# Optimization experiments

Measured on AMD Instinct MI355X. Metric: run time of the kernel, lower is better.

## Reference

```python
import math
import jax, jax.numpy as jnp
import numpy as np

EPS = 1e-5
RATIO = 0.5


def gcn_conv(x, src, dst, ew, W, b):
    # GCNConv(add_self_loops=True, normalize=True, improved=True): self-loop fill = 2.0
    N = x.shape[0]
    h = x @ W  # [N, Cout]
    deg = jax.ops.segment_sum(ew, dst, num_segments=N) + 2.0
    dinv = jnp.where(deg > 0, deg ** -0.5, 0.0)
    norm = dinv[src] * ew * dinv[dst]  # [E]
    agg = jax.ops.segment_sum(h[src] * norm[:, None], dst, num_segments=N)
    return agg + (2.0 * dinv * dinv)[:, None] * h + b


def batch_norm(x, g, b):
    # training-mode BatchNorm1d over nodes (biased variance)
    mu = x.mean(0)
    var = x.var(0)
    return (x - mu) * jax.lax.rsqrt(var + EPS) * g + b


def topk_pool(x, src, dst, ew, p):
    # TopKPooling: score = tanh(x.p/||p||), keep top ceil(ratio*N), x' = x[perm]*score[perm]
    N = x.shape[0]
    k = int(math.ceil(RATIO * N))
    score = jnp.tanh((x @ p) / jnp.linalg.norm(p))
    vals, perm = jax.lax.top_k(score, k)
    xk = x[perm] * vals[:, None]
    new_idx = jnp.full((N,), -1, jnp.int32).at[perm].set(jnp.arange(k, dtype=jnp.int32))
    ns, nd = new_idx[src], new_idx[dst]
    keep = (ns >= 0) & (nd >= 0)
    # keep fixed edge count; dropped edges get weight 0 -> contribute nothing
    return xk, jnp.where(keep, ns, 0), jnp.where(keep, nd, 0), jnp.where(keep, ew, 0.0), perm


def encode(x, src, dst, ew, mW, mb, g1, b1, cW, cb, g2, b2):
    x = batch_norm(jax.nn.relu(x @ mW + mb), g1, b1)  # MLP: Lin -> ReLU -> BN
    x = gcn_conv(x, src, dst, ew, cW, cb)
    return jax.nn.relu(batch_norm(x, g2, b2))


def unet(x, edge_src, edge_dst,
         e0_mlp_W, e0_mlp_b, e0_bn1_g, e0_bn1_b, e0_conv_W, e0_conv_b, e0_n_g, e0_n_b,
         e1_p, e1_mlp_W, e1_mlp_b, e1_bn1_g, e1_bn1_b, e1_conv_W, e1_conv_b, e1_n_g, e1_n_b,
         e2_p, e2_mlp_W, e2_mlp_b, e2_bn1_g, e2_bn1_b, e2_conv_W, e2_conv_b, e2_n_g, e2_n_b,
         d2_W, d2_b, d1_W, d1_b, d0_W, d0_b):
    E = edge_src.shape[0]
    ew0 = jnp.ones((E,), x.dtype)
    # encoder0 (no pool)
    x1 = encode(x, edge_src, edge_dst, ew0, e0_mlp_W, e0_mlp_b, e0_bn1_g, e0_bn1_b,
                e0_conv_W, e0_conv_b, e0_n_g, e0_n_b)
    # encoder1 (pool 0.5)
    xp, s1, t1, ew1, perm1 = topk_pool(x1, edge_src, edge_dst, ew0, e1_p)
    x2 = encode(xp, s1, t1, ew1, e1_mlp_W, e1_mlp_b, e1_bn1_g, e1_bn1_b,
                e1_conv_W, e1_conv_b, e1_n_g, e1_n_b)
    # encoder2 (pool 0.5)
    xp, s2, t2, ew2, perm2 = topk_pool(x2, s1, t1, ew1, e2_p)
    x3 = encode(xp, s2, t2, ew2, e2_mlp_W, e2_mlp_b, e2_bn1_g, e2_bn1_b,
                e2_conv_W, e2_conv_b, e2_n_g, e2_n_b)
    # decoder2 + unpool into x2 via perm2: up[perm]=(x+res[perm])/2, up[~perm]=res
    d = jax.nn.relu(gcn_conv(x3, s2, t2, ew2, d2_W, d2_b))
    xu = x2.at[perm2].set((d + x2[perm2]) * 0.5)
    # decoder1 + unpool into x1 via perm1
    d = jax.nn.relu(gcn_conv(xu, s1, t1, ew1, d1_W, d1_b))
    xu = x1.at[perm1].set((d + x1[perm1]) * 0.5)
    # decoder0 on the original graph, no activation
    return gcn_conv(xu, edge_src, edge_dst, ew0, d0_W, d0_b)


def setup_inputs() -> dict:
    key = jax.random.key(0)
    N, E, C = 100000, 1600000, [16, 64, 128, 256]
    ks = iter(jax.random.split(key, 64))
    nk = lambda: next(ks)

    def glorot(shape):
        s = math.sqrt(6.0 / (shape[0] + shape[1]))
        return jax.random.uniform(nk(), shape, minval=-s, maxval=s, dtype=jnp.float32)

    inp = {
        'x': jax.random.normal(nk(), (N, C[0]), jnp.float32),
        'edge_src': jax.random.randint(nk(), (E,), 0, N, jnp.int32),
        'edge_dst': jax.random.randint(nk(), (E,), 0, N, jnp.int32),
    }
    for i, (ci, co) in enumerate(zip(C[:-1], C[1:])):
        pre = f'e{i}_'
        if i > 0:
            inp[pre + 'p'] = jax.random.normal(nk(), (ci,), jnp.float32)
        inp[pre + 'mlp_W'] = glorot((ci, co)); inp[pre + 'mlp_b'] = jnp.zeros((co,), jnp.float32)
        inp[pre + 'bn1_g'] = jnp.ones((co,), jnp.float32); inp[pre + 'bn1_b'] = jnp.zeros((co,), jnp.float32)
        inp[pre + 'conv_W'] = glorot((co, co)); inp[pre + 'conv_b'] = jnp.zeros((co,), jnp.float32)
        inp[pre + 'n_g'] = jnp.ones((co,), jnp.float32); inp[pre + 'n_b'] = jnp.zeros((co,), jnp.float32)
    inp['d2_W'] = glorot((256, 128)); inp['d2_b'] = jnp.zeros((128,), jnp.float32)
    inp['d1_W'] = glorot((128, 64)); inp['d1_b'] = jnp.zeros((64,), jnp.float32)
    inp['d0_W'] = glorot((64, 16)); inp['d0_b'] = jnp.zeros((16,), jnp.float32)
    return inp


def reference(x, edge_src, edge_dst,
              e0_mlp_W, e0_mlp_b, e0_bn1_g, e0_bn1_b, e0_conv_W, e0_conv_b, e0_n_g, e0_n_b,
              e1_p, e1_mlp_W, e1_mlp_b, e1_bn1_g, e1_bn1_b, e1_conv_W, e1_conv_b, e1_n_g, e1_n_b,
              e2_p, e2_mlp_W, e2_mlp_b, e2_bn1_g, e2_bn1_b, e2_conv_W, e2_conv_b, e2_n_g, e2_n_b,
              d2_W, d2_b, d1_W, d1_b, d0_W, d0_b):
    return unet(x, edge_src, edge_dst,
                e0_mlp_W, e0_mlp_b, e0_bn1_g, e0_bn1_b, e0_conv_W, e0_conv_b, e0_n_g, e0_n_b,
                e1_p, e1_mlp_W, e1_mlp_b, e1_bn1_g, e1_bn1_b, e1_conv_W, e1_conv_b, e1_n_g, e1_n_b,
                e2_p, e2_mlp_W, e2_mlp_b, e2_bn1_g, e2_bn1_b, e2_conv_W, e2_conv_b, e2_n_g, e2_n_b,
                d2_W, d2_b, d1_W, d1_b, d0_W, d0_b)
```

## Files before the change

### kernel.cpp

```cpp
#include <hip/hip_runtime.h>
#include <math.h>

static inline int cdiv(int a, int b){ return (a + b - 1) / b; }

#define SCAN_CHUNK 4096
#define BCHUNK 4096

typedef _Float16 v4h __attribute__((ext_vector_type(4)));
typedef float    v4f __attribute__((ext_vector_type(4)));


__global__ void k_count0(const int* __restrict__ dst, int* __restrict__ cnt, int E){
  int i = blockIdx.x*blockDim.x + threadIdx.x;
  if (i < E) atomicAdd(&cnt[dst[i]], 1);
}

__global__ __launch_bounds__(256) void k_bucket(const int* __restrict__ src, const int* __restrict__ dst,
                        int E, int* __restrict__ gcur, unsigned int* __restrict__ bout){
  __shared__ int lcnt[256], gbase[256];
  int t = threadIdx.x;
  lcnt[t] = 0;
  __syncthreads();
  int base = blockIdx.x*BCHUNK;
  int end = min(base + BCHUNK, E);
  for (int i = base + t; i < end; i += 256) atomicAdd(&lcnt[dst[i] >> 9], 1);
  __syncthreads();
  gbase[t] = lcnt[t] ? atomicAdd(&gcur[t], lcnt[t]) : 0;
  __syncthreads();
  lcnt[t] = 0;
  __syncthreads();
  for (int i = base + t; i < end; i += 256){
    int s = src[i], d = dst[i];
    int b = d >> 9;
    int pos = gbase[b] + atomicAdd(&lcnt[b], 1);
    bout[pos] = ((unsigned int)s << 9) | (unsigned int)(d & 511);
  }
}

__global__ __launch_bounds__(256) void k_fill_b(const unsigned int* __restrict__ bout,
                        const int* __restrict__ rowptr, int* __restrict__ fillg,
                        int* __restrict__ cols, int N, int BPB){
  int b = blockIdx.x / BPB, sub = blockIdx.x % BPB;
  int r0 = b << 9;
  int r1 = min(r0 + 512, N);
  int start = rowptr[r0], end = rowptr[r1];
  for (int i = start + sub*256 + threadIdx.x; i < end; i += BPB*256){
    unsigned int v = bout[i];
    int d = r0 + (int)(v & 511u);
    int pos = rowptr[d] + atomicAdd(&fillg[d], 1);
    cols[pos] = (int)(v >> 9);
  }
}

__global__ void k_count_csr(const int* __restrict__ rowptrA, const int* __restrict__ colsA,
                            const int* __restrict__ nidx, int* __restrict__ cnt, int NA){
  int n = blockIdx.x*blockDim.x + threadIdx.x;
  if (n >= NA) return;
  int m = nidx[n];
  if (m < 0) return;
  int c = 0;
  int je = rowptrA[n+1];
  for (int j = rowptrA[n]; j < je; ++j) c += (nidx[colsA[j]] >= 0);
  cnt[m] = c;
}

__global__ void k_fill_csr(const int* __restrict__ rowptrA, const int* __restrict__ colsA,
                           const int* __restrict__ nidx, const int* __restrict__ rowptrB,
                           int* __restrict__ colsB, int NA){
  int n = blockIdx.x*blockDim.x + threadIdx.x;
  if (n >= NA) return;
  int m = nidx[n];
  if (m < 0) return;
  int pos = rowptrB[m];
  int je = rowptrA[n+1];
  for (int j = rowptrA[n]; j < je; ++j){
    int s = nidx[colsA[j]];
    if (s >= 0) colsB[pos++] = s;
  }
}


__global__ __launch_bounds__(256) void k_scan_p1(const int* __restrict__ in, int nIn, int* __restrict__ bsum){
  __shared__ int sh[256];
  int base = blockIdx.x*SCAN_CHUNK;
  int end = min(base + SCAN_CHUNK, nIn);
  int s = 0;
  for (int i = base + threadIdx.x; i < end; i += 256) s += in[i];
  sh[threadIdx.x] = s; __syncthreads();
  for (int o = 128; o > 0; o >>= 1){
    if (threadIdx.x < o) sh[threadIdx.x] += sh[threadIdx.x + o];
    __syncthreads();
  }
  if (threadIdx.x == 0) bsum[blockIdx.x] = sh[0];
}

__global__ __launch_bounds__(256) void k_scan_p2(int* __restrict__ bsum, int nb){
  __shared__ int sh[256];
  int t = threadIdx.x;
  int v = (t < nb) ? bsum[t] : 0;
  sh[t] = v; __syncthreads();
  for (int o = 1; o < 256; o <<= 1){
    int u = (t >= o) ? sh[t-o] : 0;
    __syncthreads();
    sh[t] += u;
    __syncthreads();
  }
  if (t < nb) bsum[t] = sh[t] - v;
}

__global__ __launch_bounds__(256) void k_scan_p3(const int* __restrict__ cnt, const int* __restrict__ bsum,
                        int* __restrict__ rowptr, float* __restrict__ dinv,
                        int* __restrict__ gcur, int nIn){
  int t = threadIdx.x;
  int tb = blockIdx.x*SCAN_CHUNK + t*16;
  int my[16]; int s = 0;
#pragma unroll
  for (int j = 0; j < 16; ++j){
    int i = tb + j;
    int v = (i < nIn) ? cnt[i] : 0;
    my[j] = v; s += v;
  }
  __shared__ int sh[256];
  sh[t] = s; __syncthreads();
  for (int o = 1; o < 256; o <<= 1){
    int u = (t >= o) ? sh[t-o] : 0;
    __syncthreads();
    sh[t] += u;
    __syncthreads();
  }
  int run = bsum[blockIdx.x] + sh[t] - s;
#pragma unroll
  for (int j = 0; j < 16; ++j){
    int i = tb + j;
    if (i < nIn){
      rowptr[i] = run;
      if (dinv) dinv[i] = rsqrtf((float)my[j] + 2.0f);
      if (gcur && (i & 511) == 0) gcur[i >> 9] = run;
      run += my[j];
    } else if (i == nIn){
      rowptr[nIn] = run;
    }
  }
}


__global__ void k_prep_w_el(const float* __restrict__ W, const float* __restrict__ ss,
                            _Float16* __restrict__ Whi, _Float16* __restrict__ Wlo,
                            float* __restrict__ bias2, const float* __restrict__ bias,
                            int KM, int M, int mshift, int mmask){
  int idx = blockIdx.x*256 + threadIdx.x;
  if (idx >= KM) return;
  int k = idx >> mshift, m = idx & mmask;
  float w = W[idx];
  if (ss) w *= ss[k];
  _Float16 hi = (_Float16)w;
  size_t oidx = ((size_t)(k >> 2)*M + m)*4 + (k & 3);
  Whi[oidx] = hi;
  if (Wlo) Wlo[oidx] = (_Float16)(w - (float)hi);
  if (k == 0) bias2[m] = bias ? bias[m] : 0.f;
}

__global__ void k_prep_bias(const float* __restrict__ W, const float* __restrict__ ss,
                            float* __restrict__ bias2, int K, int M){
  int m = blockIdx.x;
  int lane = threadIdx.x;
  float s = 0.f;
  for (int k = lane; k < K; k += 64) s = fmaf(ss[K + k], W[(size_t)k*M + m], s);
  for (int o = 32; o > 0; o >>= 1) s += __shfl_down(s, o, 64);
  if (lane == 0) bias2[m] = s;
}


template<int SPLIT>
__global__ __launch_bounds__(256) void k_gemm16(
    const float* __restrict__ A, const _Float16* __restrict__ Whi,
    const _Float16* __restrict__ Wlo, const float* __restrict__ bias2,
    float* __restrict__ Out32, _Float16* __restrict__ Out16,
    float* __restrict__ stats, int N, int K, int M, int relu)
{
  __shared__ float sacc[64], s2acc[64];
  int tid = threadIdx.x;
  if (stats){
    if (tid < 64){ sacc[tid] = 0.f; s2acc[tid] = 0.f; }
    __syncthreads();
  }
  int wave = tid >> 6, lane = tid & 63;
  int g = lane >> 4, r = lane & 15;
  int wrow0 = blockIdx.x*256 + wave*64;
  int col0 = blockIdx.y*64;
  int nf = (M - col0) >> 4; if (nf > 4) nf = 4;
  v4f acc[4][4];
#pragma unroll
  for (int rt = 0; rt < 4; ++rt)
#pragma unroll
    for (int c = 0; c < 4; ++c) acc[rt][c] = (v4f){0.f,0.f,0.f,0.f};

  for (int k0 = 0; k0 < K; k0 += 16){
    int kb = (k0 >> 2) + g;
    v4h bh[4], bl[4];
#pragma unroll
    for (int c = 0; c < 4; ++c){
      if (c >= nf) continue;
      size_t bidx = ((size_t)kb*M + col0 + c*16 + r)*4;
      bh[c] = *(const v4h*)&Whi[bidx];
      if (SPLIT) bl[c] = *(const v4h*)&Wlo[bidx];
    }
    v4h ah[4], al[4];
#pragma unroll
    for (int rt = 0; rt < 4; ++rt){
      int arow = wrow0 + rt*16 + r;
      if (arow < N){
        float4 av = *(const float4*)&A[(size_t)arow*K + k0 + g*4];
        float xs[4] = {av.x, av.y, av.z, av.w};
#pragma unroll
        for (int j = 0; j < 4; ++j){
          _Float16 hi = (_Float16)xs[j];
          ah[rt][j] = hi;
          if (SPLIT) al[rt][j] = (_Float16)(xs[j] - (float)hi);
        }
      } else {
#pragma unroll
        for (int j = 0; j < 4; ++j){ ah[rt][j] = (_Float16)0.f; if (SPLIT) al[rt][j] = (_Float16)0.f; }
      }
    }
#pragma unroll
    for (int rt = 0; rt < 4; ++rt){
#pragma unroll
      for (int c = 0; c < 4; ++c){
        if (c >= nf) continue;
        acc[rt][c] = __builtin_amdgcn_mfma_f32_16x16x16f16(ah[rt], bh[c], acc[rt][c], 0, 0, 0);
        if (SPLIT){
          acc[rt][c] = __builtin_amdgcn_mfma_f32_16x16x16f16(al[rt], bh[c], acc[rt][c], 0, 0, 0);
          acc[rt][c] = __builtin_amdgcn_mfma_f32_16x16x16f16(ah[rt], bl[c], acc[rt][c], 0, 0, 0);
        }
      }
    }
  }

#pragma unroll
  for (int c = 0; c < 4; ++c){
    if (c >= nf) continue;
    int col = col0 + c*16 + r;
    float bsv = bias2[col];
    float s = 0.f, s2 = 0.f;
#pragma unroll
    for (int rt = 0; rt < 4; ++rt){
#pragma unroll
      for (int i = 0; i < 4; ++i){
        int rr = wrow0 + rt*16 + g*4 + i;
        float v = acc[rt][c][i] + bsv;
        if (relu) v = fmaxf(v, 0.f);
        if (rr < N){
          if (Out32) Out32[(size_t)rr*M + col] = v;
          if (Out16) Out16[(size_t)rr*M + col] = (_Float16)v;
          s += v; s2 = fmaf(v, v, s2);
        }
      }
    }
    if (stats){
      s  += __shfl_xor(s, 16);  s  += __shfl_xor(s, 32);
      s2 += __shfl_xor(s2, 16); s2 += __shfl_xor(s2, 32);
      if (g == 0){
        atomicAdd(&sacc[c*16 + r], s);
        atomicAdd(&s2acc[c*16 + r], s2);
      }
    }
  }
  if (stats){
    __syncthreads();
    if (tid < 64 && col0 + tid < M){
      atomicAdd(&stats[col0 + tid], sacc[tid]);
      atomicAdd(&stats[M + col0 + tid], s2acc[tid]);
    }
  }
}


__global__ void k_bn_stats(const float* __restrict__ X, float* __restrict__ acc, int N, int C){
  int col = threadIdx.x % C;
  int rg  = threadIdx.x / C;
  int R   = blockDim.x / C;
  float s = 0.f, s2 = 0.f;
  for (int r = blockIdx.x*R + rg; r < N; r += gridDim.x*R){
    float v = X[(size_t)r*C + col];
    s += v; s2 += v*v;
  }
  __shared__ float sh[256], sh2[256];
  sh[threadIdx.x] = s; sh2[threadIdx.x] = s2;
  __syncthreads();
  if (rg == 0){
    for (int r = 1; r < R; ++r){ s += sh[r*C + col]; s2 += sh2[r*C + col]; }
    atomicAdd(&acc[col], s);
    atomicAdd(&acc[C + col], s2);
  }
}

__global__ void k_bn_final(const float* __restrict__ acc, const float* __restrict__ g,
                           const float* __restrict__ b, float* __restrict__ ss, int N, int C){
  int c = threadIdx.x;
  if (c >= C) return;
  float mu  = acc[c] / (float)N;
  float var = acc[C + c] / (float)N - mu*mu;
  float sc  = rsqrtf(var + 1e-5f) * g[c];
  ss[c]     = sc;
  ss[C + c] = b[c] - mu*sc;
}

__global__ void k_bn_apply(const float* __restrict__ X, float* __restrict__ Y,
                           const float* __restrict__ ss, int total, int C, int relu){
  int i = blockIdx.x*blockDim.x + threadIdx.x;
  if (i >= total) return;
  int c = i % C;
  float v = X[i]*ss[c] + ss[C + c];
  if (relu) v = fmaxf(v, 0.f);
  Y[i] = v;
}


template<int C, typename T>
__global__ void k_agg(const T* __restrict__ h, const int* __restrict__ rowptr,
                      const int* __restrict__ cols, const float* __restrict__ dinv,
                      const float* __restrict__ bias, float* __restrict__ out,
                      int N, int relu)
{
  constexpr int TPN = (C < 64) ? C : 64;
  constexpr int R = C / TPN;
  int gid  = blockIdx.x*blockDim.x + threadIdx.x;
  int node = gid / TPN;
  int lane = gid % TPN;
  if (node >= N) return;
  float di = dinv[node];
  float acc[R];
#pragma unroll
  for (int r = 0; r < R; ++r) acc[r] = 0.f;
  int j  = rowptr[node];
  int je = rowptr[node+1];
  for (; j + 4 <= je; j += 4){
    int s0 = cols[j], s1 = cols[j+1], s2 = cols[j+2], s3 = cols[j+3];
    float w0 = dinv[s0]*di, w1 = dinv[s1]*di, w2 = dinv[s2]*di, w3 = dinv[s3]*di;
#pragma unroll
    for (int r = 0; r < R; ++r){
      float h0 = (float)h[(size_t)s0*C + lane + r*TPN];
      float h1 = (float)h[(size_t)s1*C + lane + r*TPN];
      float h2 = (float)h[(size_t)s2*C + lane + r*TPN];
      float h3 = (float)h[(size_t)s3*C + lane + r*TPN];
      acc[r] = fmaf(w0, h0, acc[r]);
      acc[r] = fmaf(w1, h1, acc[r]);
      acc[r] = fmaf(w2, h2, acc[r]);
      acc[r] = fmaf(w3, h3, acc[r]);
    }
  }
  for (; j < je; ++j){
    int s = cols[j];
    float wgt = dinv[s]*di;
#pragma unroll
    for (int r = 0; r < R; ++r)
      acc[r] = fmaf(wgt, (float)h[(size_t)s*C + lane + r*TPN], acc[r]);
  }
  float sw = 2.f*di*di;
#pragma unroll
  for (int r = 0; r < R; ++r){
    int c = lane + r*TPN;
    float v = acc[r] + sw*(float)h[(size_t)node*C + c] + bias[c];
    if (relu) v = fmaxf(v, 0.f);
    out[(size_t)node*C + c] = v;
  }
}

template<typename T>
static void launch_agg(const T* h, const int* rp, const int* cl, const float* dv,
                       const float* bias, float* o, int N, int C, int relu, hipStream_t stream){
  int tpn = (C < 64) ? C : 64;
  dim3 g(cdiv(N*tpn, 256));
  switch (C){
    case 16:  k_agg<16,T> <<<g, dim3(256), 0, stream>>>(h, rp, cl, dv, bias, o, N, relu); break;
    case 64:  k_agg<64,T> <<<g, dim3(256), 0, stream>>>(h, rp, cl, dv, bias, o, N, relu); break;
    case 128: k_agg<128,T><<<g, dim3(256), 0, stream>>>(h, rp, cl, dv, bias, o, N, relu); break;
    case 256: k_agg<256,T><<<g, dim3(256), 0, stream>>>(h, rp, cl, dv, bias, o, N, relu); break;
  }
}


__global__ void k_score(const float* __restrict__ X, const float* __restrict__ p,
                        float* __restrict__ val, unsigned int* __restrict__ key, int N, int C){
  int wid  = (blockIdx.x*blockDim.x + threadIdx.x) >> 6;
  int lane = threadIdx.x & 63;
  if (wid >= N) return;
  float s = 0.f, np = 0.f;
  for (int c = lane; c < C; c += 64){
    float pv = p[c];
    s = fmaf(X[(size_t)wid*C + c], pv, s);
    np = fmaf(pv, pv, np);
  }
  for (int o = 32; o > 0; o >>= 1){ s += __shfl_down(s, o, 64); np += __shfl_down(np, o, 64); }
  if (lane == 0){
    float sc = tanhf(s * rsqrtf(np));
    val[wid] = sc;
    unsigned int b = __float_as_uint(sc);
    key[wid] = (b & 0x80000000u) ? ~b : (b | 0x80000000u);
  }
}

__global__ void k_hist_hi(const unsigned int* __restrict__ key, int N, unsigned int* __restrict__ hist){
  int i = blockIdx.x*blockDim.x + threadIdx.x;
  if (i < N) atomicAdd(&hist[key[i] >> 16], 1u);
}

__global__ void k_hist_lo(const unsigned int* __restrict__ key, int N,
                          const int* __restrict__ state, unsigned int* __restrict__ hist){
  int i = blockIdx.x*blockDim.x + threadIdx.x;
  if (i >= N) return;
  unsigned int kk = key[i];
  if ((int)(kk >> 16) == state[1]) atomicAdd(&hist[kk & 0xffffu], 1u);
}

__global__ void k_scan_hist(unsigned int* __restrict__ hist, int* __restrict__ state,
                            int karg, int kidx, int bidx, int ridx){
  __shared__ unsigned int part[1024];
  __shared__ unsigned int suff[1024];
  int t = threadIdx.x;
  unsigned int s = 0;
  int base = t*64;
  for (int j = 0; j < 64; ++j) s += hist[base + j];
  part[t] = s;
  suff[t] = s;
  __syncthreads();
  for (int o = 1; o < 1024; o <<= 1){
    unsigned int v = (t + o < 1024) ? suff[t + o] : 0u;
    __syncthreads();
    suff[t] += v;
    __syncthreads();
  }
  unsigned int k = (unsigned int)((kidx >= 0) ? state[kidx] : karg);
  unsigned int above = suff[t] - part[t];
  if (above < k && above + part[t] >= k){
    unsigned int cum = above;
    for (int b = 63; b >= 0; --b){
      unsigned int c = hist[base + b];
      if (cum + c >= k){ state[bidx] = base + b; state[ridx] = (int)(k - cum); break; }
      cum += c;
    }
  }
  __syncthreads();
  for (int j = 0; j < 64; ++j) hist[base + j] = 0u;
}


__global__ __launch_bounds__(256) void k_sel_p1(const unsigned int* __restrict__ key, int n,
                       const int* __restrict__ state, int2* __restrict__ bcnt){
  unsigned int T = ((unsigned int)state[1] << 16) | (unsigned int)state[3];
  int base = blockIdx.x*SCAN_CHUNK;
  int end = min(base + SCAN_CHUNK, n);
  int gt = 0, eq = 0;
  for (int i = base + threadIdx.x; i < end; i += 256){
    unsigned int v = key[i];
    gt += (v > T); eq += (v == T);
  }
  __shared__ int sg[256], se[256];
  sg[threadIdx.x] = gt; se[threadIdx.x] = eq;
  __syncthreads();
  for (int o = 128; o > 0; o >>= 1){
    if (threadIdx.x < o){ sg[threadIdx.x] += sg[threadIdx.x + o]; se[threadIdx.x] += se[threadIdx.x + o]; }
    __syncthreads();
  }
  if (threadIdx.x == 0) bcnt[blockIdx.x] = make_int2(sg[0], se[0]);
}

__global__ __launch_bounds__(256) void k_sel_p2(int2* __restrict__ bcnt, int nb){
  __shared__ int sg[256], se[256];
  int t = threadIdx.x;
  int2 v = (t < nb) ? bcnt[t] : make_int2(0, 0);
  sg[t] = v.x; se[t] = v.y; __syncthreads();
  for (int o = 1; o < 256; o <<= 1){
    int a = (t >= o) ? sg[t-o] : 0;
    int b = (t >= o) ? se[t-o] : 0;
    __syncthreads();
    sg[t] += a; se[t] += b;
    __syncthreads();
  }
  if (t < nb) bcnt[t] = make_int2(sg[t] - v.x, se[t] - v.y);
}

__global__ __launch_bounds__(256) void k_sel_p3(const unsigned int* __restrict__ key, int n,
                       const int* __restrict__ state, const int2* __restrict__ bcnt,
                       int* __restrict__ nidx){
  unsigned int T = ((unsigned int)state[1] << 16) | (unsigned int)state[3];
  int m = state[4];
  int t = threadIdx.x;
  int tb = blockIdx.x*SCAN_CHUNK + t*16;
  unsigned int kk[16];
  int gt = 0, eq = 0;
#pragma unroll
  for (int j = 0; j < 16; ++j){
    int i = tb + j;
    bool ok = i < n;
    unsigned int v = ok ? key[i] : 0u;
    kk[j] = v;
    gt += (ok && v > T); eq += (ok && v == T);
  }
  __shared__ unsigned long long sh[256];
  unsigned long long mine = ((unsigned long long)(unsigned)gt << 32) | (unsigned)eq;
  sh[t] = mine; __syncthreads();
  for (int o = 1; o < 256; o <<= 1){
    unsigned long long u = (t >= o) ? sh[t-o] : 0ull;
    __syncthreads();
    sh[t] += u;
    __syncthreads();
  }
  unsigned long long excl = sh[t] - mine;
  int2 bo = bcnt[blockIdx.x];
  int gb = bo.x + (int)(excl >> 32);
  int eb = bo.y + (int)(excl & 0xffffffffu);
#pragma unroll
  for (int j = 0; j < 16; ++j){
    int i = tb + j;
    if (i >= n) break;
    unsigned int v = kk[j];
    bool g = v > T, e = v == T;
    bool sel = g || (e && eb < m);
    nidx[i] = sel ? (gb + (eb < m ? eb : m)) : -1;
    gb += g; eb += e;
  }
}

__global__ void k_pool(const float* __restrict__ X, const float* __restrict__ val,
                       const int* __restrict__ nidx, float* __restrict__ Y, int N, int C){
  int i = blockIdx.x*blockDim.x + threadIdx.x;
  int n = i / C, c = i % C;
  if (n >= N) return;
  int m = nidx[n];
  if (m >= 0) Y[(size_t)m*C + c] = X[i]*val[n];
}

__global__ void k_unpool(float* __restrict__ X, const float* __restrict__ D,
                         const int* __restrict__ nidx, int N, int C){
  int i = blockIdx.x*blockDim.x + threadIdx.x;
  int n = i / C, c = i % C;
  if (n >= N) return;
  int m = nidx[n];
  if (m >= 0) X[i] = (D[(size_t)m*C + c] + X[i])*0.5f;
}


extern "C" void kernel_launch(void* const* d_in, const int* in_sizes, int n_in,
                              void* d_out, int out_size, void* d_ws, size_t ws_size,
                              hipStream_t stream)
{
  const float* x_in = (const float*)d_in[0];
  const int*   esrc = (const int*)d_in[1];
  const int*   edst = (const int*)d_in[2];
  const float* e0_mlp_W = (const float*)d_in[3];
  const float* e0_mlp_b = (const float*)d_in[4];
  const float* e0_bn1_g = (const float*)d_in[5];
  const float* e0_bn1_b = (const float*)d_in[6];
  const float* e0_conv_W= (const float*)d_in[7];
  const float* e0_conv_b= (const float*)d_in[8];
  const float* e0_n_g   = (const float*)d_in[9];
  const float* e0_n_b   = (const float*)d_in[10];
  const float* e1_p     = (const float*)d_in[11];
  const float* e1_mlp_W = (const float*)d_in[12];
  const float* e1_mlp_b = (const float*)d_in[13];
  const float* e1_bn1_g = (const float*)d_in[14];
  const float* e1_bn1_b = (const float*)d_in[15];
  const float* e1_conv_W= (const float*)d_in[16];
  const float* e1_conv_b= (const float*)d_in[17];
  const float* e1_n_g   = (const float*)d_in[18];
  const float* e1_n_b   = (const float*)d_in[19];
  const float* e2_p     = (const float*)d_in[20];
  const float* e2_mlp_W = (const float*)d_in[21];
  const float* e2_mlp_b = (const float*)d_in[22];
  const float* e2_bn1_g = (const float*)d_in[23];
  const float* e2_bn1_b = (const float*)d_in[24];
  const float* e2_conv_W= (const float*)d_in[25];
  const float* e2_conv_b= (const float*)d_in[26];
  const float* e2_n_g   = (const float*)d_in[27];
  const float* e2_n_b   = (const float*)d_in[28];
  const float* d2_W = (const float*)d_in[29];
  const float* d2_b = (const float*)d_in[30];
  const float* d1_W = (const float*)d_in[31];
  const float* d1_b = (const float*)d_in[32];
  const float* d0_W = (const float*)d_in[33];
  const float* d0_b = (const float*)d_in[34];
  float* out = (float*)d_out;

  const int N0 = in_sizes[0] / 16;
  const int E  = in_sizes[1];
  const int N1 = (N0 + 1) / 2;
  const int N2 = (N1 + 1) / 2;
  const int NB0 = cdiv(N0, 512);

  char* w = (char*)d_ws;
  auto alloc = [&](size_t b)->void*{ void* p = (void*)w; w += (b + 255) & ~(size_t)255; return p; };
  float* x1 = (float*)alloc((size_t)N0*64*4);
  float* x2 = (float*)alloc((size_t)N1*128*4);
  float* x3 = (float*)alloc((size_t)N2*256*4);
  size_t tmax = (size_t)N0*64*4;
  float* tA = (float*)alloc(tmax);
  float* tB = (float*)alloc(tmax);
  _Float16* h16 = (_Float16*)alloc((size_t)N0*64*2);
  int* rowptr0 = (int*)alloc((size_t)(N0+1)*4);
  int* rowptr1 = (int*)alloc((size_t)(N1+1)*4);
  int* rowptr2 = (int*)alloc((size_t)(N2+1)*4);
  int* cnt  = (int*)alloc((size_t)(N0+1)*4);
  int* fillg = (int*)alloc((size_t)N0*4);
  int* cols0 = (int*)alloc((size_t)E*4);
  int* cols1 = (int*)alloc((size_t)E*4);
  int* cols2 = (int*)alloc((size_t)E*4);
  float* dinv0 = (float*)alloc((size_t)N0*4);
  float* dinv1 = (float*)alloc((size_t)N1*4);
  float* dinv2 = (float*)alloc((size_t)N2*4);
  int* nidx1 = (int*)alloc((size_t)N0*4);
  int* nidx2 = (int*)alloc((size_t)N1*4);
  float* val = (float*)alloc((size_t)N0*4);
  unsigned int* key = (unsigned int*)alloc((size_t)N0*4);
  unsigned int* hist = (unsigned int*)alloc((size_t)65536*4);
  int* state = (int*)alloc(64);
  int* bsum = (int*)alloc(1024*4);
  int2* bcnt = (int2*)alloc(1024*8);
  int* gcur = (int*)alloc(256*4);
  float* bnacc = (float*)alloc(512*4);
  float* ss = (float*)alloc(512*4);
  _Float16* whi = (_Float16*)alloc((size_t)256*256*2);
  _Float16* wlo = (_Float16*)alloc((size_t)256*256*2);
  float* bias2 = (float*)alloc(256*4);
  if ((size_t)(w - (char*)d_ws) > ws_size) return;
  unsigned int* bout = (unsigned int*)tA;

  auto run_prep = [&](const float* W, const float* bias, int K, int M, int split){
    int KM = K*M;
    k_prep_w_el<<<dim3(cdiv(KM,256)), dim3(256), 0, stream>>>(
        W, nullptr, whi, split ? wlo : nullptr, bias2, bias, KM, M, __builtin_ctz(M), M-1);
  };
  auto run_prep_bn = [&](const float* W, const float* g, const float* b, int Ncount, int K, int M, int split){
    k_bn_final<<<dim3(1), dim3(K), 0, stream>>>(bnacc, g, b, ss, Ncount, K);
    int KM = K*M;
    k_prep_w_el<<<dim3(cdiv(KM,256)), dim3(256), 0, stream>>>(
        W, ss, whi, split ? wlo : nullptr, bias2, nullptr, KM, M, __builtin_ctz(M), M-1);
    k_prep_bias<<<dim3(M), dim3(64), 0, stream>>>(W, ss, bias2, K, M);
  };
  auto run_gemm = [&](const float* A, float* O32, _Float16* O16, float* stats,
                      int N, int K, int M, int act, int split){
    dim3 grd(cdiv(N,256), cdiv(M,64));
    if (split)
      k_gemm16<1><<<grd, dim3(256), 0, stream>>>(A, whi, wlo, bias2, O32, O16, stats, N, K, M, act);
    else
      k_gemm16<0><<<grd, dim3(256), 0, stream>>>(A, whi, wlo, bias2, O32, O16, stats, N, K, M, act);
  };
  auto run_scan = [&](const int* in, int* rowptr, float* dinv, int* gc, int nIn){
    int nb = cdiv(nIn + 1, SCAN_CHUNK);
    k_scan_p1<<<dim3(nb), dim3(256), 0, stream>>>(in, nIn, bsum);
    k_scan_p2<<<dim3(1), dim3(256), 0, stream>>>(bsum, nb);
    k_scan_p3<<<dim3(nb), dim3(256), 0, stream>>>(in, bsum, rowptr, dinv, gc, nIn);
  };
  auto run_topk = [&](const float* X, const float* p, int N, int C, int k, int* nidx){
    k_score<<<dim3(cdiv(N*64,256)), dim3(256), 0, stream>>>(X, p, val, key, N, C);
    k_hist_hi<<<dim3(cdiv(N,256)), dim3(256), 0, stream>>>(key, N, hist);
    k_scan_hist<<<dim3(1), dim3(1024), 0, stream>>>(hist, state, k, -1, 1, 2);
    k_hist_lo<<<dim3(cdiv(N,256)), dim3(256), 0, stream>>>(key, N, state, hist);
    k_scan_hist<<<dim3(1), dim3(1024), 0, stream>>>(hist, state, 0, 2, 3, 4);
    int nb = cdiv(N, SCAN_CHUNK);
    k_sel_p1<<<dim3(nb), dim3(256), 0, stream>>>(key, N, state, bcnt);
    k_sel_p2<<<dim3(1), dim3(256), 0, stream>>>(bcnt, nb);
    k_sel_p3<<<dim3(nb), dim3(256), 0, stream>>>(key, N, state, bcnt, nidx);
  };

  hipMemsetAsync(hist, 0, 65536*4, stream);

  hipMemsetAsync(cnt, 0, (size_t)(N0+1)*4, stream);
  k_count0<<<dim3(cdiv(E,256)), dim3(256), 0, stream>>>(edst, cnt, E);
  run_scan(cnt, rowptr0, dinv0, gcur, N0);
  k_bucket<<<dim3(cdiv(E,BCHUNK)), dim3(256), 0, stream>>>(esrc, edst, E, gcur, bout);
  hipMemsetAsync(fillg, 0, (size_t)N0*4, stream);
  k_fill_b<<<dim3(NB0*4), dim3(256), 0, stream>>>(bout, rowptr0, fillg, cols0, N0, 4);

  hipMemsetAsync(bnacc, 0, 2*64*4, stream);
  run_prep(e0_mlp_W, e0_mlp_b, 16, 64, 1);
  run_gemm(x_in, tA, nullptr, bnacc, N0, 16, 64, 1, 1);
  run_prep_bn(e0_conv_W, e0_bn1_g, e0_bn1_b, N0, 64, 64, 1);
  run_gemm(tA, tB, nullptr, nullptr, N0, 64, 64, 0, 1);
  launch_agg<float>(tB, rowptr0, cols0, dinv0, e0_conv_b, tA, N0, 64, 0, stream);
  hipMemsetAsync(bnacc, 0, 2*64*4, stream);
  k_bn_stats<<<dim3(256), dim3(256), 0, stream>>>(tA, bnacc, N0, 64);
  k_bn_final<<<dim3(1), dim3(64), 0, stream>>>(bnacc, e0_n_g, e0_n_b, ss, N0, 64);
  k_bn_apply<<<dim3(cdiv(N0*64,256)), dim3(256), 0, stream>>>(tA, x1, ss, N0*64, 64, 1);

  run_topk(x1, e1_p, N0, 64, N1, nidx1);
  k_pool<<<dim3(cdiv(N0*64,256)), dim3(256), 0, stream>>>(x1, val, nidx1, tA, N0, 64);
  k_count_csr<<<dim3(cdiv(N0,256)), dim3(256), 0, stream>>>(rowptr0, cols0, nidx1, cnt, N0);
  run_scan(cnt, rowptr1, dinv1, nullptr, N1);
  k_fill_csr<<<dim3(cdiv(N0,256)), dim3(256), 0, stream>>>(rowptr0, cols0, nidx1, rowptr1, cols1, N0);

  hipMemsetAsync(bnacc, 0, 2*128*4, stream);
  run_prep(e1_mlp_W, e1_mlp_b, 64, 128, 1);
  run_gemm(tA, tB, nullptr, bnacc, N1, 64, 128, 1, 1);
  run_prep_bn(e1_conv_W, e1_bn1_g, e1_bn1_b, N1, 128, 128, 1);
  run_gemm(tB, tA, nullptr, nullptr, N1, 128, 128, 0, 1);
  launch_agg<float>(tA, rowptr1, cols1, dinv1, e1_conv_b, tB, N1, 128, 0, stream);
  hipMemsetAsync(bnacc, 0, 2*128*4, stream);
  k_bn_stats<<<dim3(256), dim3(256), 0, stream>>>(tB, bnacc, N1, 128);
  k_bn_final<<<dim3(1), dim3(128), 0, stream>>>(bnacc, e1_n_g, e1_n_b, ss, N1, 128);
  k_bn_apply<<<dim3(cdiv(N1*128,256)), dim3(256), 0, stream>>>(tB, x2, ss, N1*128, 128, 1);

  run_topk(x2, e2_p, N1, 128, N2, nidx2);
  k_pool<<<dim3(cdiv(N1*128,256)), dim3(256), 0, stream>>>(x2, val, nidx2, tA, N1, 128);
  k_count_csr<<<dim3(cdiv(N1,256)), dim3(256), 0, stream>>>(rowptr1, cols1, nidx2, cnt, N1);
  run_scan(cnt, rowptr2, dinv2, nullptr, N2);
  k_fill_csr<<<dim3(cdiv(N1,256)), dim3(256), 0, stream>>>(rowptr1, cols1, nidx2, rowptr2, cols2, N1);

  hipMemsetAsync(bnacc, 0, 2*256*4, stream);
  run_prep(e2_mlp_W, e2_mlp_b, 128, 256, 0);
  run_gemm(tA, tB, nullptr, bnacc, N2, 128, 256, 1, 0);
  run_prep_bn(e2_conv_W, e2_bn1_g, e2_bn1_b, N2, 256, 256, 0);
  run_gemm(tB, nullptr, h16, nullptr, N2, 256, 256, 0, 0);
  launch_agg<_Float16>(h16, rowptr2, cols2, dinv2, e2_conv_b, tB, N2, 256, 0, stream);
  hipMemsetAsync(bnacc, 0, 2*256*4, stream);
  k_bn_stats<<<dim3(256), dim3(256), 0, stream>>>(tB, bnacc, N2, 256);
  k_bn_final<<<dim3(1), dim3(256), 0, stream>>>(bnacc, e2_n_g, e2_n_b, ss, N2, 256);
  k_bn_apply<<<dim3(cdiv(N2*256,256)), dim3(256), 0, stream>>>(tB, x3, ss, N2*256, 256, 1);

  run_prep(d2_W, nullptr, 256, 128, 0);
  run_gemm(x3, nullptr, h16, nullptr, N2, 256, 128, 0, 0);
  launch_agg<_Float16>(h16, rowptr2, cols2, dinv2, d2_b, tB, N2, 128, 1, stream);
  k_unpool<<<dim3(cdiv(N1*128,256)), dim3(256), 0, stream>>>(x2, tB, nidx2, N1, 128);

  run_prep(d1_W, nullptr, 128, 64, 0);
  run_gemm(x2, nullptr, h16, nullptr, N1, 128, 64, 0, 0);
  launch_agg<_Float16>(h16, rowptr1, cols1, dinv1, d1_b, tB, N1, 64, 1, stream);
  k_unpool<<<dim3(cdiv(N0*64,256)), dim3(256), 0, stream>>>(x1, tB, nidx1, N0, 64);

  run_prep(d0_W, nullptr, 64, 16, 0);
  run_gemm(x1, nullptr, h16, nullptr, N0, 64, 16, 0, 0);
  launch_agg<_Float16>(h16, rowptr0, cols0, dinv0, d0_b, out, N0, 16, 0, stream);
}
```

Baseline: 1.247 ms.

## Fuse BN-apply with top-k scoring, gather pooled rows in GEMM, parallelize CSR derivation

Merges the final BatchNorm apply and ReLU with the top-k score computation so the encoder output is not re-read for scoring. Drops the separate pooling kernel: top-k selection now writes a perm array, and the next GEMM gathers rows through perm and scales them by the score. Pooled CSR construction uses 16-lane ballot compaction into a temporary buffer plus a copy kernel, replacing one-thread-per-node serial loops. Aggregation processes channel pairs per thread with wider loads, which reduces thread count and raises bytes per load. The GEMM A reads become indirect gathers, which may coalesce less well.

Measured after the change: 1.194 ms. 1.04x faster.

```diff
diff --git a/kernel.cpp b/kernel.cpp
--- a/kernel.cpp
+++ b/kernel.cpp
@@ -8,6 +8,7 @@
 
 typedef _Float16 v4h __attribute__((ext_vector_type(4)));
 typedef float    v4f __attribute__((ext_vector_type(4)));
+typedef _Float16 h2  __attribute__((ext_vector_type(2)));
 
 
 __global__ void k_count0(const int* __restrict__ dst, int* __restrict__ cnt, int E){
@@ -52,31 +53,44 @@
   }
 }
 
-__global__ void k_count_csr(const int* __restrict__ rowptrA, const int* __restrict__ colsA,
-                            const int* __restrict__ nidx, int* __restrict__ cnt, int NA){
-  int n = blockIdx.x*blockDim.x + threadIdx.x;
-  if (n >= NA) return;
-  int m = nidx[n];
+
+__global__ __launch_bounds__(256) void k_csr_keep(const int* __restrict__ rowptrA, const int* __restrict__ colsA,
+                         const int* __restrict__ nidx, int* __restrict__ tmp,
+                         int* __restrict__ cnt, int NA){
+  int t = threadIdx.x;
+  int g = (blockIdx.x*256 + t) >> 4;
+  int lane = t & 15;
+  if (g >= NA) return;
+  int m = nidx[g];
   if (m < 0) return;
-  int c = 0;
-  int je = rowptrA[n+1];
-  for (int j = rowptrA[n]; j < je; ++j) c += (nidx[colsA[j]] >= 0);
-  cnt[m] = c;
-}
-
-__global__ void k_fill_csr(const int* __restrict__ rowptrA, const int* __restrict__ colsA,
-                           const int* __restrict__ nidx, const int* __restrict__ rowptrB,
-                           int* __restrict__ colsB, int NA){
-  int n = blockIdx.x*blockDim.x + threadIdx.x;
-  if (n >= NA) return;
-  int m = nidx[n];
+  int jb = rowptrA[g], je = rowptrA[g+1];
+  int run = 0;
+  int shift = (t & 63) & ~15;
+  for (int j0 = jb; j0 < je; j0 += 16){
+    int j = j0 + lane;
+    int s = -1;
+    if (j < je) s = nidx[colsA[j]];
+    bool keep = s >= 0;
+    unsigned long long bal = __ballot(keep);
+    unsigned int gm = (unsigned int)(bal >> shift) & 0xFFFFu;
+    if (keep) tmp[jb + run + __popc(gm & ((1u << lane) - 1))] = s;
+    run += __popc(gm);
+  }
+  if (lane == 0) cnt[m] = run;
+}
+
+__global__ __launch_bounds__(256) void k_csr_copy(const int* __restrict__ rowptrA, const int* __restrict__ nidx,
+                         const int* __restrict__ tmp, const int* __restrict__ rowptrB,
+                         int* __restrict__ colsB, int NA){
+  int t = threadIdx.x;
+  int g = (blockIdx.x*256 + t) >> 4;
+  int lane = t & 15;
+  if (g >= NA) return;
+  int m = nidx[g];
   if (m < 0) return;
-  int pos = rowptrB[m];
-  int je = rowptrA[n+1];
-  for (int j = rowptrA[n]; j < je; ++j){
-    int s = nidx[colsA[j]];
-    if (s >= 0) colsB[pos++] = s;
-  }
+  int jbA = rowptrA[g];
+  int db = rowptrB[m], n = rowptrB[m+1] - db;
+  for (int j = lane; j < n; j += 16) colsB[db + j] = tmp[jbA + j];
 }
 
 
@@ -176,7 +190,8 @@
     const float* __restrict__ A, const _Float16* __restrict__ Whi,
     const _Float16* __restrict__ Wlo, const float* __restrict__ bias2,
     float* __restrict__ Out32, _Float16* __restrict__ Out16,
-    float* __restrict__ stats, int N, int K, int M, int relu)
+    float* __restrict__ stats, const int* __restrict__ permA,
+    const float* __restrict__ valA, int N, int K, int M, int relu)
 {
   __shared__ float sacc[64], s2acc[64];
   int tid = threadIdx.x;
@@ -189,6 +204,18 @@
   int wrow0 = blockIdx.x*256 + wave*64;
   int col0 = blockIdx.y*64;
   int nf = (M - col0) >> 4; if (nf > 4) nf = 4;
+
+  int srow[4]; float sclr[4];
+#pragma unroll
+  for (int rt = 0; rt < 4; ++rt){
+    int arow = wrow0 + rt*16 + r;
+    if (arow < N){
+      int sr = permA ? permA[arow] : arow;
+      srow[rt] = sr;
+      sclr[rt] = permA ? valA[sr] : 1.f;
+    } else { srow[rt] = -1; sclr[rt] = 0.f; }
+  }
+
   v4f acc[4][4];
 #pragma unroll
   for (int rt = 0; rt < 4; ++rt)
@@ -208,10 +235,9 @@
     v4h ah[4], al[4];
 #pragma unroll
     for (int rt = 0; rt < 4; ++rt){
-      int arow = wrow0 + rt*16 + r;
-      if (arow < N){
-        float4 av = *(const float4*)&A[(size_t)arow*K + k0 + g*4];
-        float xs[4] = {av.x, av.y, av.z, av.w};
+      if (srow[rt] >= 0){
+        float4 av = *(const float4*)&A[(size_t)srow[rt]*K + k0 + g*4];
+        float xs[4] = {av.x*sclr[rt], av.y*sclr[rt], av.z*sclr[rt], av.w*sclr[rt]};
 #pragma unroll
         for (int j = 0; j < 4; ++j){
           _Float16 hi = (_Float16)xs[j];
@@ -316,6 +342,39 @@
   Y[i] = v;
 }
 
+__global__ void k_bnap_score(const float* __restrict__ X, float* __restrict__ Y,
+                             const float* __restrict__ ss, const float* __restrict__ p,
+                             float* __restrict__ val, unsigned int* __restrict__ key,
+                             int N, int C){
+  int wid  = (blockIdx.x*blockDim.x + threadIdx.x) >> 6;
+  int lane = threadIdx.x & 63;
+  if (wid >= N) return;
+  float s = 0.f, np = 0.f;
+  for (int c = lane; c < C; c += 64){
+    float v = X[(size_t)wid*C + c]*ss[c] + ss[C + c];
+    v = fmaxf(v, 0.f);
+    Y[(size_t)wid*C + c] = v;
+    float pv = p[c];
+    s = fmaf(v, pv, s);
+    np = fmaf(pv, pv, np);
+  }
+  for (int o = 32; o > 0; o >>= 1){ s += __shfl_down(s, o, 64); np += __shfl_down(np, o, 64); }
+  if (lane == 0){
+    float sc = tanhf(s * rsqrtf(np));
+    val[wid] = sc;
+    unsigned int b = __float_as_uint(sc);
+    key[wid] = (b & 0x80000000u) ? ~b : (b | 0x80000000u);
+  }
+}
+
+
+__device__ inline float2 ldpair(const float* h, size_t off){
+  return *(const float2*)(h + off);
+}
+__device__ inline float2 ldpair(const _Float16* h, size_t off){
+  h2 v = *(const h2*)(h + off);
+  return make_float2((float)v[0], (float)v[1]);
+}
 
 template<int C, typename T>
 __global__ void k_agg(const T* __restrict__ h, const int* __restrict__ rowptr,
@@ -323,16 +382,17 @@
                       const float* __restrict__ bias, float* __restrict__ out,
                       int N, int relu)
 {
-  constexpr int TPN = (C < 64) ? C : 64;
-  constexpr int R = C / TPN;
+  constexpr int PAIRS = C/2;
+  constexpr int TPN = (PAIRS < 64) ? PAIRS : 64;
+  constexpr int R = PAIRS / TPN;
   int gid  = blockIdx.x*blockDim.x + threadIdx.x;
   int node = gid / TPN;
   int lane = gid % TPN;
   if (node >= N) return;
   float di = dinv[node];
-  float acc[R];
-#pragma unroll
-  for (int r = 0; r < R; ++r) acc[r] = 0.f;
+  float2 acc[R];
+#pragma unroll
+  for (int r = 0; r < R; ++r) acc[r] = make_float2(0.f, 0.f);
   int j  = rowptr[node];
   int je = rowptr[node+1];
   for (; j + 4 <= je; j += 4){
@@ -340,37 +400,44 @@
     float w0 = dinv[s0]*di, w1 = dinv[s1]*di, w2 = dinv[s2]*di, w3 = dinv[s3]*di;
 #pragma unroll
     for (int r = 0; r < R; ++r){
-      float h0 = (float)h[(size_t)s0*C + lane + r*TPN];
-      float h1 = (float)h[(size_t)s1*C + lane + r*TPN];
-      float h2 = (float)h[(size_t)s2*C + lane + r*TPN];
-      float h3 = (float)h[(size_t)s3*C + lane + r*TPN];
-      acc[r] = fmaf(w0, h0, acc[r]);
-      acc[r] = fmaf(w1, h1, acc[r]);
-      acc[r] = fmaf(w2, h2, acc[r]);
-      acc[r] = fmaf(w3, h3, acc[r]);
+      size_t po = (size_t)(lane + r*TPN)*2;
+      float2 h0 = ldpair(h, (size_t)s0*C + po);
+      float2 h1 = ldpair(h, (size_t)s1*C + po);
+      float2 h2v = ldpair(h, (size_t)s2*C + po);
+      float2 h3 = ldpair(h, (size_t)s3*C + po);
+      acc[r].x = fmaf(w0, h0.x, acc[r].x); acc[r].y = fmaf(w0, h0.y, acc[r].y);
+      acc[r].x = fmaf(w1, h1.x, acc[r].x); acc[r].y = fmaf(w1, h1.y, acc[r].y);
+      acc[r].x = fmaf(w2, h2v.x, acc[r].x); acc[r].y = fmaf(w2, h2v.y, acc[r].y);
+      acc[r].x = fmaf(w3, h3.x, acc[r].x); acc[r].y = fmaf(w3, h3.y, acc[r].y);
     }
   }
   for (; j < je; ++j){
     int s = cols[j];
     float wgt = dinv[s]*di;
 #pragma unroll
-    for (int r = 0; r < R; ++r)
-      acc[r] = fmaf(wgt, (float)h[(size_t)s*C + lane + r*TPN], acc[r]);
+    for (int r = 0; r < R; ++r){
+      float2 hv = ldpair(h, (size_t)s*C + (size_t)(lane + r*TPN)*2);
+      acc[r].x = fmaf(wgt, hv.x, acc[r].x);
+      acc[r].y = fmaf(wgt, hv.y, acc[r].y);
+    }
   }
   float sw = 2.f*di*di;
 #pragma unroll
   for (int r = 0; r < R; ++r){
-    int c = lane + r*TPN;
-    float v = acc[r] + sw*(float)h[(size_t)node*C + c] + bias[c];
-    if (relu) v = fmaxf(v, 0.f);
-    out[(size_t)node*C + c] = v;
+    int pc = (lane + r*TPN)*2;
+    float2 hv = ldpair(h, (size_t)node*C + pc);
+    float2 v;
+    v.x = acc[r].x + sw*hv.x + bias[pc];
+    v.y = acc[r].y + sw*hv.y + bias[pc+1];
+    if (relu){ v.x = fmaxf(v.x, 0.f); v.y = fmaxf(v.y, 0.f); }
+    *(float2*)&out[(size_t)node*C + pc] = v;
   }
 }
 
 template<typename T>
 static void launch_agg(const T* h, const int* rp, const int* cl, const float* dv,
                        const float* bias, float* o, int N, int C, int relu, hipStream_t stream){
-  int tpn = (C < 64) ? C : 64;
+  int tpn = (C/2 < 64) ? C/2 : 64;
   dim3 g(cdiv(N*tpn, 256));
   switch (C){
     case 16:  k_agg<16,T> <<<g, dim3(256), 0, stream>>>(h, rp, cl, dv, bias, o, N, relu); break;
@@ -380,26 +447,6 @@
   }
 }
 
-
-__global__ void k_score(const float* __restrict__ X, const float* __restrict__ p,
-                        float* __restrict__ val, unsigned int* __restrict__ key, int N, int C){
-  int wid  = (blockIdx.x*blockDim.x + threadIdx.x) >> 6;
-  int lane = threadIdx.x & 63;
-  if (wid >= N) return;
-  float s = 0.f, np = 0.f;
-  for (int c = lane; c < C; c += 64){
-    float pv = p[c];
-    s = fmaf(X[(size_t)wid*C + c], pv, s);
-    np = fmaf(pv, pv, np);
-  }
-  for (int o = 32; o > 0; o >>= 1){ s += __shfl_down(s, o, 64); np += __shfl_down(np, o, 64); }
-  if (lane == 0){
-    float sc = tanhf(s * rsqrtf(np));
-    val[wid] = sc;
-    unsigned int b = __float_as_uint(sc);
-    key[wid] = (b & 0x80000000u) ? ~b : (b | 0x80000000u);
-  }
-}
 
 __global__ void k_hist_hi(const unsigned int* __restrict__ key, int N, unsigned int* __restrict__ hist){
   int i = blockIdx.x*blockDim.x + threadIdx.x;
@@ -445,7 +492,6 @@
   for (int j = 0; j < 64; ++j) hist[base + j] = 0u;
 }
 
-
 __global__ __launch_bounds__(256) void k_sel_p1(const unsigned int* __restrict__ key, int n,
                        const int* __restrict__ state, int2* __restrict__ bcnt){
   unsigned int T = ((unsigned int)state[1] << 16) | (unsigned int)state[3];
@@ -483,7 +529,7 @@
 
 __global__ __launch_bounds__(256) void k_sel_p3(const unsigned int* __restrict__ key, int n,
                        const int* __restrict__ state, const int2* __restrict__ bcnt,
-                       int* __restrict__ nidx){
+                       int* __restrict__ nidx, int* __restrict__ perm){
   unsigned int T = ((unsigned int)state[1] << 16) | (unsigned int)state[3];
   int m = state[4];
   int t = threadIdx.x;
@@ -518,18 +564,13 @@
     unsigned int v = kk[j];
     bool g = v > T, e = v == T;
     bool sel = g || (e && eb < m);
-    nidx[i] = sel ? (gb + (eb < m ? eb : m)) : -1;
+    if (sel){
+      int ni = gb + (eb < m ? eb : m);
+      nidx[i] = ni;
+      perm[ni] = i;
+    } else nidx[i] = -1;
     gb += g; eb += e;
   }
-}
-
-__global__ void k_pool(const float* __restrict__ X, const float* __restrict__ val,
-                       const int* __restrict__ nidx, float* __restrict__ Y, int N, int C){
-  int i = blockIdx.x*blockDim.x + threadIdx.x;
-  int n = i / C, c = i % C;
-  if (n >= N) return;
-  int m = nidx[n];
-  if (m >= 0) Y[(size_t)m*C + c] = X[i]*val[n];
 }
 
 __global__ void k_unpool(float* __restrict__ X, const float* __restrict__ D,
@@ -611,6 +652,8 @@
   float* dinv2 = (float*)alloc((size_t)N2*4);
   int* nidx1 = (int*)alloc((size_t)N0*4);
   int* nidx2 = (int*)alloc((size_t)N1*4);
+  int* perm1 = (int*)alloc((size_t)N1*4);
+  int* perm2 = (int*)alloc((size_t)N2*4);
   float* val = (float*)alloc((size_t)N0*4);
   unsigned int* key = (unsigned int*)alloc((size_t)N0*4);
   unsigned int* hist = (unsigned int*)alloc((size_t)65536*4);
@@ -625,6 +668,7 @@
   float* bias2 = (float*)alloc(256*4);
   if ((size_t)(w - (char*)d_ws) > ws_size) return;
   unsigned int* bout = (unsigned int*)tA;
+  int* tmpE = (int*)tA;
 
   auto run_prep = [&](const float* W, const float* bias, int K, int M, int split){
     int KM = K*M;
@@ -639,12 +683,12 @@
     k_prep_bias<<<dim3(M), dim3(64), 0, stream>>>(W, ss, bias2, K, M);
   };
   auto run_gemm = [&](const float* A, float* O32, _Float16* O16, float* stats,
-                      int N, int K, int M, int act, int split){
+                      const int* perm, int N, int K, int M, int act, int split){
     dim3 grd(cdiv(N,256), cdiv(M,64));
     if (split)
-      k_gemm16<1><<<grd, dim3(256), 0, stream>>>(A, whi, wlo, bias2, O32, O16, stats, N, K, M, act);
+      k_gemm16<1><<<grd, dim3(256), 0, stream>>>(A, whi, wlo, bias2, O32, O16, stats, perm, val, N, K, M, act);
     else
-      k_gemm16<0><<<grd, dim3(256), 0, stream>>>(A, whi, wlo, bias2, O32, O16, stats, N, K, M, act);
+      k_gemm16<0><<<grd, dim3(256), 0, stream>>>(A, whi, wlo, bias2, O32, O16, stats, perm, val, N, K, M, act);
   };
   auto run_scan = [&](const int* in, int* rowptr, float* dinv, int* gc, int nIn){
     int nb = cdiv(nIn + 1, SCAN_CHUNK);
@@ -652,8 +696,7 @@
     k_scan_p2<<<dim3(1), dim3(256), 0, stream>>>(bsum, nb);
     k_scan_p3<<<dim3(nb), dim3(256), 0, stream>>>(in, bsum, rowptr, dinv, gc, nIn);
   };
-  auto run_topk = [&](const float* X, const float* p, int N, int C, int k, int* nidx){
-    k_score<<<dim3(cdiv(N*64,256)), dim3(256), 0, stream>>>(X, p, val, key, N, C);
+  auto run_topk_rest = [&](int N, int k, int* nidx, int* perm){
     k_hist_hi<<<dim3(cdiv(N,256)), dim3(256), 0, stream>>>(key, N, hist);
     k_scan_hist<<<dim3(1), dim3(1024), 0, stream>>>(hist, state, k, -1, 1, 2);
     k_hist_lo<<<dim3(cdiv(N,256)), dim3(256), 0, stream>>>(key, N, state, hist);
@@ -661,7 +704,13 @@
     int nb = cdiv(N, SCAN_CHUNK);
     k_sel_p1<<<dim3(nb), dim3(256), 0, stream>>>(key, N, state, bcnt);
     k_sel_p2<<<dim3(1), dim3(256), 0, stream>>>(bcnt, nb);
-    k_sel_p3<<<dim3(nb), dim3(256), 0, stream>>>(key, N, state, bcnt, nidx);
+    k_sel_p3<<<dim3(nb), dim3(256), 0, stream>>>(key, N, state, bcnt, nidx, perm);
+  };
+  auto run_csr_derive = [&](const int* rpA, const int* clA, const int* nidx,
+                            int* rpB, int* clB, float* dvB, int NA, int NB){
+    k_csr_keep<<<dim3(cdiv(NA*16,256)), dim3(256), 0, stream>>>(rpA, clA, nidx, tmpE, cnt, NA);
+    run_scan(cnt, rpB, dvB, nullptr, NB);
+    k_csr_copy<<<dim3(cdiv(NA*16,256)), dim3(256), 0, stream>>>(rpA, nidx, tmpE, rpB, clB, NA);
   };
 
   hipMemsetAsync(hist, 0, 65536*4, stream);
@@ -675,43 +724,37 @@
 
   hipMemsetAsync(bnacc, 0, 2*64*4, stream);
   run_prep(e0_mlp_W, e0_mlp_b, 16, 64, 1);
-  run_gemm(x_in, tA, nullptr, bnacc, N0, 16, 64, 1, 1);
+  run_gemm(x_in, tA, nullptr, bnacc, nullptr, N0, 16, 64, 1, 1);
   run_prep_bn(e0_conv_W, e0_bn1_g, e0_bn1_b, N0, 64, 64, 1);
-  run_gemm(tA, tB, nullptr, nullptr, N0, 64, 64, 0, 1);
+  run_gemm(tA, tB, nullptr, nullptr, nullptr, N0, 64, 64, 0, 1);
   launch_agg<float>(tB, rowptr0, cols0, dinv0, e0_conv_b, tA, N0, 64, 0, stream);
   hipMemsetAsync(bnacc, 0, 2*64*4, stream);
   k_bn_stats<<<dim3(256), dim3(256), 0, stream>>>(tA, bnacc, N0, 64);
   k_bn_final<<<dim3(1), dim3(64), 0, stream>>>(bnacc, e0_n_g, e0_n_b, ss, N0, 64);
-  k_bn_apply<<<dim3(cdiv(N0*64,256)), dim3(256), 0, stream>>>(tA, x1, ss, N0*64, 64, 1);
-
-  run_topk(x1, e1_p, N0, 64, N1, nidx1);
-  k_pool<<<dim3(cdiv(N0*64,256)), dim3(256), 0, stream>>>(x1, val, nidx1, tA, N0, 64);
-  k_count_csr<<<dim3(cdiv(N0,256)), dim3(256), 0, stream>>>(rowptr0, cols0, nidx1, cnt, N0);
-  run_scan(cnt, rowptr1, dinv1, nullptr, N1);
-  k_fill_csr<<<dim3(cdiv(N0,256)), dim3(256), 0, stream>>>(rowptr0, cols0, nidx1, rowptr1, cols1, N0);
+  k_bnap_score<<<dim3(cdiv(N0*64,256)), dim3(256), 0, stream>>>(tA, x1, ss, e1_p, val, key, N0, 64);
+
+  run_topk_rest(N0, N1, nidx1, perm1);
+  run_csr_derive(rowptr0, cols0, nidx1, rowptr1, cols1, dinv1, N0, N1);
 
   hipMemsetAsync(bnacc, 0, 2*128*4, stream);
   run_prep(e1_mlp_W, e1_mlp_b, 64, 128, 1);
-  run_gemm(tA, tB, nullptr, bnacc, N1, 64, 128, 1, 1);
+  run_gemm(x1, tB, nullptr, bnacc, perm1, N1, 64, 128, 1, 1);
   run_prep_bn(e1_conv_W, e1_bn1_g, e1_bn1_b, N1, 128, 128, 1);
-  run_gemm(tB, tA, nullptr, nullptr, N1, 128, 128, 0, 1);
+  run_gemm(tB, tA, nullptr, nullptr, nullptr, N1, 128, 128, 0, 1);
   launch_agg<float>(tA, rowptr1, cols1, dinv1, e1_conv_b, tB, N1, 128, 0, stream);
   hipMemsetAsync(bnacc, 0, 2*128*4, stream);
   k_bn_stats<<<dim3(256), dim3(256), 0, stream>>>(tB, bnacc, N1, 128);
   k_bn_final<<<dim3(1), dim3(128), 0, stream>>>(bnacc, e1_n_g, e1_n_b, ss, N1, 128);
-  k_bn_apply<<<dim3(cdiv(N1*128,256)), dim3(256), 0, stream>>>(tB, x2, ss, N1*128, 128, 1);
-
-  run_topk(x2, e2_p, N1, 128, N2, nidx2);
-  k_pool<<<dim3(cdiv(N1*128,256)), dim3(256), 0, stream>>>(x2, val, nidx2, tA, N1, 128);
-  k_count_csr<<<dim3(cdiv(N1,256)), dim3(256), 0, stream>>>(rowptr1, cols1, nidx2, cnt, N1);
-  run_scan(cnt, rowptr2, dinv2, nullptr, N2);
-  k_fill_csr<<<dim3(cdiv(N1,256)), dim3(256), 0, stream>>>(rowptr1, cols1, nidx2, rowptr2, cols2, N1);
+  k_bnap_score<<<dim3(cdiv(N1*64,256)), dim3(256), 0, stream>>>(tB, x2, ss, e2_p, val, key, N1, 128);
+
+  run_topk_rest(N1, N2, nidx2, perm2);
+  run_csr_derive(rowptr1, cols1, nidx2, rowptr2, cols2, dinv2, N1, N2);
 
   hipMemsetAsync(bnacc, 0, 2*256*4, stream);
   run_prep(e2_mlp_W, e2_mlp_b, 128, 256, 0);
-  run_gemm(tA, tB, nullptr, bnacc, N2, 128, 256, 1, 0);
+  run_gemm(x2, tB, nullptr, bnacc, perm2, N2, 128, 256, 1, 0);
   run_prep_bn(e2_conv_W, e2_bn1_g, e2_bn1_b, N2, 256, 256, 0);
-  run_gemm(tB, nullptr, h16, nullptr, N2, 256, 256, 0, 0);
+  run_gemm(tB, nullptr, h16, nullptr, nullptr, N2, 256, 256, 0, 0);
   launch_agg<_Float16>(h16, rowptr2, cols2, dinv2, e2_conv_b, tB, N2, 256, 0, stream);
   hipMemsetAsync(bnacc, 0, 2*256*4, stream);
   k_bn_stats<<<dim3(256), dim3(256), 0, stream>>>(tB, bnacc, N2, 256);
@@ -719,16 +762,16 @@
   k_bn_apply<<<dim3(cdiv(N2*256,256)), dim3(256), 0, stream>>>(tB, x3, ss, N2*256, 256, 1);
 
   run_prep(d2_W, nullptr, 256, 128, 0);
-  run_gemm(x3, nullptr, h16, nullptr, N2, 256, 128, 0, 0);
+  run_gemm(x3, nullptr, h16, nullptr, nullptr, N2, 256, 128, 0, 0);
   launch_agg<_Float16>(h16, rowptr2, cols2, dinv2, d2_b, tB, N2, 128, 1, stream);
   k_unpool<<<dim3(cdiv(N1*128,256)), dim3(256), 0, stream>>>(x2, tB, nidx2, N1, 128);
 
   run_prep(d1_W, nullptr, 128, 64, 0);
-  run_gemm(x2, nullptr, h16, nullptr, N1, 128, 64, 0, 0);
+  run_gemm(x2, nullptr, h16, nullptr, nullptr, N1, 128, 64, 0, 0);
   launch_agg<_Float16>(h16, rowptr1, cols1, dinv1, d1_b, tB, N1, 64, 1, stream);
   k_unpool<<<dim3(cdiv(N0*64,256)), dim3(256), 0, stream>>>(x1, tB, nidx1, N0, 64);
 
   run_prep(d0_W, nullptr, 64, 16, 0);
-  run_gemm(x1, nullptr, h16, nullptr, N0, 64, 16, 0, 0);
+  run_gemm(x1, nullptr, h16, nullptr, nullptr, N0, 64, 16, 0, 0);
   launch_agg<_Float16>(h16, rowptr0, cols0, dinv0, d0_b, out, N0, 16, 0, stream);
 }
```
